# Optimization experiments

Measured on AMD Instinct MI355X. Metric: run time of the kernel, lower is better.

## Reference

```python
import jax, jax.numpy as jnp
import numpy as np

SIZE = 512
FEATURES = 16
IN_FEATURES = 16
BATCH = 8192
EXCLUSIVE = 1  # module init arg exclusive=True


def setup_inputs() -> dict:
    key = jax.random.key(0)
    k1, k2, k3, k4 = jax.random.split(key, 4)
    inputs = jax.random.normal(k1, (BATCH, IN_FEATURES), dtype=jnp.float32)
    cache = jax.random.normal(k2, (BATCH, SIZE, IN_FEATURES), dtype=jnp.float32)
    kernel = jax.random.normal(k3, (SIZE * IN_FEATURES, SIZE * FEATURES), dtype=jnp.float32)
    bias = jax.random.normal(k4, (SIZE, FEATURES), dtype=jnp.float32)
    index = 300
    return {"inputs": inputs, "cache": cache, "kernel": kernel, "bias": bias, "index": index}


def reference(inputs, cache, kernel, bias, index):
    # Faithful translation of FastMaskedDense1D.update_site.
    batch, in_features = inputs.shape
    size, features = bias.shape
    size_i = index + 1

    # scatter the new input site into the cache (index - exclusive >= 0 branch)
    if index - EXCLUSIVE >= 0:
        cache = cache.at[:, index - EXCLUSIVE, :].set(inputs)

    # cached inputs up to the current site, flattened: (batch, size_i*in_features)
    cache_i = cache[:, :size_i, :].reshape(batch, size_i * in_features)

    # dynamic slice of the kernel for output site `index`: (size_i, in_features, features)
    kernel_i = kernel.reshape(size, in_features, size, features)[:size_i, :, index, :]

    # triu(ones, exclusive) kron ones mask, sliced at [:size_i, :, index, :]:
    # row j is 1 iff index >= j + exclusive
    mask = (jnp.arange(size_i) <= index - EXCLUSIVE).astype(kernel_i.dtype)
    kernel_i = (kernel_i * mask[:, None, None]).reshape(size_i * in_features, features)

    y_i = cache_i @ kernel_i + bias[index, :]  # (batch, features)
    return y_i
```

## Files before the change

### kernel.cpp

```cpp
#include <hip/hip_runtime.h>


#define EXCLUSIVE 1
#define SIZEV     512
#define NF        16
#define NIF       16
#define KROW      (SIZEV * NF)
#define CROW      (SIZEV * NIF)
#define MB        16
#define KC        128
#define SA        136
#define SK        20

__device__ __forceinline__ void fma4(float4& a, float s, float4 b) {
    a.x = fmaf(s, b.x, a.x);
    a.y = fmaf(s, b.y, a.y);
    a.z = fmaf(s, b.z, a.z);
    a.w = fmaf(s, b.w, a.w);
}

__device__ __forceinline__ float4 red4(float4 v, int m) {
    v.x += __shfl_xor(v.x, m, 64);
    v.y += __shfl_xor(v.y, m, 64);
    v.z += __shfl_xor(v.z, m, 64);
    v.w += __shfl_xor(v.w, m, 64);
    return v;
}

__global__ __launch_bounds__(256) void pack_k(
    const float* __restrict__ kern,
    const int*   __restrict__ idxp,
    float*       __restrict__ kp)
{
    const int index = *idxp;
    const int jc = index - EXCLUSIVE + 1;
    const int KT = (jc > 0) ? jc * NIF : 0;
    const int KTpad = (KT + KC - 1) & ~(KC - 1);
    const int t  = blockIdx.x * blockDim.x + threadIdx.x;
    const int r  = t >> 2;
    const int q  = t & 3;
    if (r < KTpad) {
        float4 v = {0.f, 0.f, 0.f, 0.f};
        if (r < KT)
            v = *(const float4*)(kern + (size_t)r * KROW + (size_t)index * NF + 4 * q);
        *(float4*)(kp + (size_t)r * NF + 4 * q) = v;
    }
}

__global__ __launch_bounds__(512) void fmd_kernel(
    const float* __restrict__ inputs,
    const float* __restrict__ cache,
    const float* __restrict__ kp,
    const float* __restrict__ bias,
    const int*   __restrict__ idxp,
    float*       __restrict__ out)
{
    __shared__ float A [2][MB * SA];
    __shared__ float Kl[2][KC * SK];
    __shared__ float Red[MB * NF];

    const int index = *idxp;
    const int jc = index - EXCLUSIVE + 1;
    const int KM = (jc > 0) ? (jc - 1) * NIF : 0;
    const int NC = (KM + KC - 1) / KC;

    const int tid  = threadIdx.x;
    const int lane = tid & 63;
    const int w    = tid >> 6;
    const int kq   = lane & 15;
    const int rq   = lane >> 4;
    const int fh   = w & 1;
    const int rh   = (w >> 1) & 1;
    const int ks   = w >> 2;
    const int row0 = blockIdx.x * MB;

    const int lr0 = rh * 8 + rq;
    const int lr1 = lr0 + 4;

    const int arow = tid >> 5;
    const int ac4  = tid & 31;
    const int krow = tid >> 2;
    const int kc4  = tid & 3;

    float4 acc00 = {0,0,0,0}, acc01 = {0,0,0,0};
    float4 acc10 = {0,0,0,0}, acc11 = {0,0,0,0};

    const float4* cvec = (const float4*)cache;
    const float4* kpv  = (const float4*)kp;

    float4 stA, stK;

    if (NC > 0) {
        stA = cvec[(size_t)(row0 + arow) * (CROW/4) + ac4];
        stK = kpv[4 * krow + kc4];
        *(float4*)&A [0][arow * SA + 4 * ac4] = stA;
        *(float4*)&Kl[0][krow * SK + 4 * kc4] = stK;

        for (int c = 0; c < NC; ++c) {
            const int k0 = c * KC;
            if (c + 1 < NC) {
                stA = cvec[(size_t)(row0 + arow) * (CROW/4) + ((k0 + KC) >> 2) + ac4];
                stK = kpv[4 * (k0 + KC + krow) + kc4];
            }
            __syncthreads();

            const int buf  = c & 1;
            const int kend = min(KC, KM - k0);
            const int nt   = (kend - 16 * ks + 31) >> 5;
            const float* Ab = &A [buf][0];
            const float* Kb = &Kl[buf][0];

            #pragma unroll 4
            for (int t = 0; t < nt; ++t) {
                const int kk = kq + 32 * t + 16 * ks;
                float a0 = Ab[lr0 * SA + kk];
                float a1 = Ab[lr1 * SA + kk];
                const float* kp4 = &Kb[kk * SK + fh * 8];
                float4 kv0 = *(const float4*)kp4;
                float4 kv1 = *(const float4*)(kp4 + 4);
                fma4(acc00, a0, kv0); fma4(acc01, a0, kv1);
                fma4(acc10, a1, kv0); fma4(acc11, a1, kv1);
            }

            if (c + 1 < NC) {
                const int b2 = (c + 1) & 1;
                *(float4*)&A [b2][arow * SA + 4 * ac4] = stA;
                *(float4*)&Kl[b2][krow * SK + 4 * kc4] = stK;
            }
        }
    }

    if (jc > 0 && ks == 0) {
        const float* kg = kp + (size_t)((jc - 1) * NIF + kq) * NF + fh * 8;
        float4 kv0 = *(const float4*)kg;
        float4 kv1 = *(const float4*)(kg + 4);
        float in0 = inputs[(size_t)(row0 + lr0) * NIF + kq];
        float in1 = inputs[(size_t)(row0 + lr1) * NIF + kq];
        fma4(acc00, in0, kv0); fma4(acc01, in0, kv1);
        fma4(acc10, in1, kv0); fma4(acc11, in1, kv1);
    }

    #pragma unroll
    for (int m = 1; m <= 8; m <<= 1) {
        acc00 = red4(acc00, m); acc01 = red4(acc01, m);
        acc10 = red4(acc10, m); acc10 = acc10; acc11 = red4(acc11, m);
    }

    const int rp = kq >> 1;
    const int qp = kq & 1;
    float4 v = (rp == 0) ? (qp == 0 ? acc00 : acc01)
                         : (qp == 0 ? acc10 : acc11);
    const int brow = lr0 + 4 * rp;
    const int fcol = fh * 8 + 4 * qp;

    if (ks == 1 && kq < 4)
        *(float4*)&Red[brow * NF + fcol] = v;
    __syncthreads();
    if (ks == 0 && kq < 4) {
        float4 o  = *(const float4*)&Red[brow * NF + fcol];
        float4 b4 = *(const float4*)&bias[(size_t)index * NF + fcol];
        v.x += o.x + b4.x; v.y += o.y + b4.y;
        v.z += o.z + b4.z; v.w += o.w + b4.w;
        *(float4*)&out[(size_t)(row0 + brow) * NF + fcol] = v;
    }
}

extern "C" void kernel_launch(void* const* d_in, const int* in_sizes, int n_in,
                              void* d_out, int out_size, void* d_ws, size_t ws_size,
                              hipStream_t stream) {
    const float* inputs = (const float*)d_in[0];
    const float* cache  = (const float*)d_in[1];
    const float* kern   = (const float*)d_in[2];
    const float* bias   = (const float*)d_in[3];
    const int*   idxp   = (const int*)d_in[4];
    float*       out    = (float*)d_out;
    float*       kp     = (float*)d_ws;

    const int batch = in_sizes[0] / NIF;
    const int grid  = batch / MB;

    pack_k<<<(SIZEV * NIF * 4) / 256, 256, 0, stream>>>(kern, idxp, kp);
    fmd_kernel<<<grid, 512, 0, stream>>>(inputs, cache, kp, bias, idxp, out);
}
```

Measured before the change: 438.1 us.

## Load cache activations directly into registers and widen per-thread output tile

```diff
diff --git a/kernel.cpp b/kernel.cpp
--- a/kernel.cpp
+++ b/kernel.cpp
@@ -8,9 +8,9 @@
 #define KROW      (SIZEV * NF)
 #define CROW      (SIZEV * NIF)
 #define MB        16
-#define KC        128
-#define SA        136
+#define KCH       256
 #define SK        20
+#define NW        8
 
 __device__ __forceinline__ void fma4(float4& a, float s, float4 b) {
     a.x = fmaf(s, b.x, a.x);
@@ -35,7 +35,7 @@
     const int index = *idxp;
     const int jc = index - EXCLUSIVE + 1;
     const int KT = (jc > 0) ? jc * NIF : 0;
-    const int KTpad = (KT + KC - 1) & ~(KC - 1);
+    const int KTpad = (KT + KCH - 1) & ~(KCH - 1);
     const int t  = blockIdx.x * blockDim.x + threadIdx.x;
     const int r  = t >> 2;
     const int q  = t & 3;
@@ -47,7 +47,7 @@
     }
 }
 
-__global__ __launch_bounds__(512) void fmd_kernel(
+__global__ __launch_bounds__(512, 4) void fmd_kernel(
     const float* __restrict__ inputs,
     const float* __restrict__ cache,
     const float* __restrict__ kp,
@@ -55,113 +55,143 @@
     const int*   __restrict__ idxp,
     float*       __restrict__ out)
 {
-    __shared__ float A [2][MB * SA];
-    __shared__ float Kl[2][KC * SK];
-    __shared__ float Red[MB * NF];
+    __shared__ float Kl[2][KCH * SK];
+    __shared__ float Red[NW * MB * NF];
 
     const int index = *idxp;
     const int jc = index - EXCLUSIVE + 1;
     const int KM = (jc > 0) ? (jc - 1) * NIF : 0;
-    const int NC = (KM + KC - 1) / KC;
+    const int NC = (KM + KCH - 1) / KCH;
 
     const int tid  = threadIdx.x;
     const int lane = tid & 63;
-    const int w    = tid >> 6;
+    const int ks   = tid >> 6;
     const int kq   = lane & 15;
     const int rq   = lane >> 4;
-    const int fh   = w & 1;
-    const int rh   = (w >> 1) & 1;
-    const int ks   = w >> 2;
     const int row0 = blockIdx.x * MB;
 
-    const int lr0 = rh * 8 + rq;
-    const int lr1 = lr0 + 4;
-
-    const int arow = tid >> 5;
-    const int ac4  = tid & 31;
-    const int krow = tid >> 2;
-    const int kc4  = tid & 3;
-
-    float4 acc00 = {0,0,0,0}, acc01 = {0,0,0,0};
-    float4 acc10 = {0,0,0,0}, acc11 = {0,0,0,0};
-
-    const float4* cvec = (const float4*)cache;
-    const float4* kpv  = (const float4*)kp;
-
-    float4 stA, stK;
+    const int srow = tid >> 1;
+    const int sq   = (tid & 1) * 2;
+
+    float4 acc[4][4];
+    #pragma unroll
+    for (int r = 0; r < 4; ++r)
+        #pragma unroll
+        for (int q = 0; q < 4; ++q)
+            acc[r][q] = make_float4(0.f, 0.f, 0.f, 0.f);
+
+    const float4* kpv = (const float4*)kp;
+    const float* Abase = cache + (size_t)(row0 + rq * 4) * CROW + kq + 16 * ks;
+
+    float4 st0, st1;
+    float  aR[2][4], aN[2][4];
 
     if (NC > 0) {
-        stA = cvec[(size_t)(row0 + arow) * (CROW/4) + ac4];
-        stK = kpv[4 * krow + kc4];
-        *(float4*)&A [0][arow * SA + 4 * ac4] = stA;
-        *(float4*)&Kl[0][krow * SK + 4 * kc4] = stK;
+        st0 = kpv[(size_t)4 * srow + sq];
+        st1 = kpv[(size_t)4 * srow + sq + 1];
+        *(float4*)&Kl[0][srow * SK + 4 * sq]       = st0;
+        *(float4*)&Kl[0][srow * SK + 4 * (sq + 1)] = st1;
+        #pragma unroll
+        for (int t = 0; t < 2; ++t)
+            #pragma unroll
+            for (int r = 0; r < 4; ++r)
+                aR[t][r] = Abase[(size_t)r * CROW + 128 * t];
 
         for (int c = 0; c < NC; ++c) {
-            const int k0 = c * KC;
+            const int k0 = c * KCH;
             if (c + 1 < NC) {
-                stA = cvec[(size_t)(row0 + arow) * (CROW/4) + ((k0 + KC) >> 2) + ac4];
-                stK = kpv[4 * (k0 + KC + krow) + kc4];
+                const int kn = k0 + KCH;
+                st0 = kpv[(size_t)4 * (kn + srow) + sq];
+                st1 = kpv[(size_t)4 * (kn + srow) + sq + 1];
+                #pragma unroll
+                for (int t = 0; t < 2; ++t)
+                    #pragma unroll
+                    for (int r = 0; r < 4; ++r)
+                        aN[t][r] = Abase[(size_t)r * CROW + kn + 128 * t];
             }
             __syncthreads();
 
             const int buf  = c & 1;
-            const int kend = min(KC, KM - k0);
-            const int nt   = (kend - 16 * ks + 31) >> 5;
-            const float* Ab = &A [buf][0];
+            const int kend = min(KCH, KM - k0);
             const float* Kb = &Kl[buf][0];
 
-            #pragma unroll 4
-            for (int t = 0; t < nt; ++t) {
-                const int kk = kq + 32 * t + 16 * ks;
-                float a0 = Ab[lr0 * SA + kk];
-                float a1 = Ab[lr1 * SA + kk];
-                const float* kp4 = &Kb[kk * SK + fh * 8];
-                float4 kv0 = *(const float4*)kp4;
-                float4 kv1 = *(const float4*)(kp4 + 4);
-                fma4(acc00, a0, kv0); fma4(acc01, a0, kv1);
-                fma4(acc10, a1, kv0); fma4(acc11, a1, kv1);
+            #pragma unroll
+            for (int t = 0; t < 2; ++t) {
+                const int sb = 16 * ks + 128 * t;
+                if (sb < kend) {
+                    const float* Kp = Kb + (kq + sb) * SK;
+                    float4 kv0 = *(const float4*)(Kp);
+                    float4 kv1 = *(const float4*)(Kp + 4);
+                    float4 kv2 = *(const float4*)(Kp + 8);
+                    float4 kv3 = *(const float4*)(Kp + 12);
+                    #pragma unroll
+                    for (int r = 0; r < 4; ++r) {
+                        const float a = aR[t][r];
+                        fma4(acc[r][0], a, kv0);
+                        fma4(acc[r][1], a, kv1);
+                        fma4(acc[r][2], a, kv2);
+                        fma4(acc[r][3], a, kv3);
+                    }
+                }
             }
 
             if (c + 1 < NC) {
                 const int b2 = (c + 1) & 1;
-                *(float4*)&A [b2][arow * SA + 4 * ac4] = stA;
-                *(float4*)&Kl[b2][krow * SK + 4 * kc4] = stK;
+                *(float4*)&Kl[b2][srow * SK + 4 * sq]       = st0;
+                *(float4*)&Kl[b2][srow * SK + 4 * (sq + 1)] = st1;
+                #pragma unroll
+                for (int t = 0; t < 2; ++t)
+                    #pragma unroll
+                    for (int r = 0; r < 4; ++r)
+                        aR[t][r] = aN[t][r];
             }
         }
     }
 
     if (jc > 0 && ks == 0) {
-        const float* kg = kp + (size_t)((jc - 1) * NIF + kq) * NF + fh * 8;
-        float4 kv0 = *(const float4*)kg;
+        const float* kg = kp + (size_t)((jc - 1) * NIF + kq) * NF;
+        float4 kv0 = *(const float4*)(kg);
         float4 kv1 = *(const float4*)(kg + 4);
-        float in0 = inputs[(size_t)(row0 + lr0) * NIF + kq];
-        float in1 = inputs[(size_t)(row0 + lr1) * NIF + kq];
-        fma4(acc00, in0, kv0); fma4(acc01, in0, kv1);
-        fma4(acc10, in1, kv0); fma4(acc11, in1, kv1);
+        float4 kv2 = *(const float4*)(kg + 8);
+        float4 kv3 = *(const float4*)(kg + 12);
+        #pragma unroll
+        for (int r = 0; r < 4; ++r) {
+            const float a = inputs[(size_t)(row0 + rq * 4 + r) * NIF + kq];
+            fma4(acc[r][0], a, kv0);
+            fma4(acc[r][1], a, kv1);
+            fma4(acc[r][2], a, kv2);
+            fma4(acc[r][3], a, kv3);
+        }
     }
 
     #pragma unroll
-    for (int m = 1; m <= 8; m <<= 1) {
-        acc00 = red4(acc00, m); acc01 = red4(acc01, m);
-        acc10 = red4(acc10, m); acc10 = acc10; acc11 = red4(acc11, m);
-    }
-
-    const int rp = kq >> 1;
-    const int qp = kq & 1;
-    float4 v = (rp == 0) ? (qp == 0 ? acc00 : acc01)
-                         : (qp == 0 ? acc10 : acc11);
-    const int brow = lr0 + 4 * rp;
-    const int fcol = fh * 8 + 4 * qp;
-
-    if (ks == 1 && kq < 4)
-        *(float4*)&Red[brow * NF + fcol] = v;
+    for (int m = 1; m <= 8; m <<= 1)
+        #pragma unroll
+        for (int r = 0; r < 4; ++r)
+            #pragma unroll
+            for (int q = 0; q < 4; ++q)
+                acc[r][q] = red4(acc[r][q], m);
+
+    float4 v = acc[0][0];
+    #pragma unroll
+    for (int r = 0; r < 4; ++r)
+        #pragma unroll
+        for (int q = 0; q < 4; ++q)
+            if ((kq >> 2) == r && (kq & 3) == q) v = acc[r][q];
+    {
+        const int row  = rq * 4 + (kq >> 2);
+        const int quad = kq & 3;
+        *(float4*)&Red[ks * (MB * NF) + row * NF + 4 * quad] = v;
+    }
     __syncthreads();
-    if (ks == 0 && kq < 4) {
-        float4 o  = *(const float4*)&Red[brow * NF + fcol];
-        float4 b4 = *(const float4*)&bias[(size_t)index * NF + fcol];
-        v.x += o.x + b4.x; v.y += o.y + b4.y;
-        v.z += o.z + b4.z; v.w += o.w + b4.w;
-        *(float4*)&out[(size_t)(row0 + brow) * NF + fcol] = v;
+
+    if (tid < MB * NF) {
+        const int f = tid & 15;
+        float s = bias[(size_t)index * NF + f];
+        #pragma unroll
+        for (int ww = 0; ww < NW; ++ww)
+            s += Red[ww * (MB * NF) + tid];
+        out[(size_t)row0 * NF + tid] = s;
     }
 }
 
```

After: 442.9 us. No clear change (+1.1%).
